# Kernel optimization log

Measured on AMD Instinct MI355X. Metric: run time of the kernel, lower is better.

The kernel has to match this reference:

```python
import jax, jax.numpy as jnp
import numpy as np

V, E, H, S, B = 32000, 512, 1024, 256, 128
D_WIN = 5.0  # local attention half-window D


def setup_inputs() -> dict:
    key = jax.random.key(0)
    ks = jax.random.split(key, 12)
    f32 = jnp.float32
    nrm = lambda k, shape, s=0.02: (s * jax.random.normal(k, shape, dtype=f32))
    x = jax.random.randint(ks[0], (1, B), 0, V)  # single decode step of token ids
    previous_hidden = jax.random.normal(ks[1], (1, B, H), dtype=f32)
    encoder_outputs = jax.random.normal(ks[2], (S, B, H), dtype=f32)
    lengths = jax.random.randint(ks[3], (B,), S // 2, S + 1)
    enc_masks = (jnp.arange(S)[:, None] < lengths[None, :]).astype(jnp.int32)  # (S,B)
    emb = nrm(ks[4], (V, E))
    W_dec = nrm(ks[5], (H, H)); b_dec = jnp.zeros((H,), f32)
    W_pos = nrm(ks[6], (H, H)); b_pos = jnp.zeros((H,), f32)
    w_proj = nrm(ks[7], (1, H))
    W_ih = nrm(ks[8], (3 * H, E + H)); b_ih = jnp.zeros((3 * H,), f32)
    W_hh = nrm(ks[9], (3 * H, H)); b_hh = jnp.zeros((3 * H,), f32)
    W_fc = nrm(ks[10], (V, E + 2 * H)); b_fc = jnp.zeros((V,), f32)
    return dict(x=x, previous_hidden=previous_hidden, encoder_outputs=encoder_outputs,
                enc_masks=enc_masks, emb=emb, W_dec=W_dec, b_dec=b_dec,
                W_pos=W_pos, b_pos=b_pos, w_proj=w_proj,
                W_ih=W_ih, b_ih=b_ih, W_hh=W_hh, b_hh=b_hh, W_fc=W_fc, b_fc=b_fc)


def reference(x, previous_hidden, encoder_outputs, enc_masks, emb, W_dec, b_dec,
              W_pos, b_pos, w_proj, W_ih, b_ih, W_hh, b_hh, W_fc, b_fc):
    src_len = encoder_outputs.shape[0]
    x_emb = emb[x]                                   # (1,B,E); dropout is eval-mode identity
    phd = previous_hidden[-1]                        # (B,H)

    # per-batch encoder lengths: first index where mask==0, 0 -> full length
    src_lens = jnp.argmin(enc_masks.T, axis=1)
    src_lens = jnp.where(src_lens == 0, src_len, src_lens).astype(jnp.float32)  # (B,)

    # local (Luong-style) alignment scores: tanh of dot(dec, enc)
    dw = phd @ W_dec.T + b_dec                       # (B,H)
    energy = jnp.tanh(jnp.einsum('bh,sbh->sb', dw, encoder_outputs))  # (S,B)
    scores = jnp.where(enc_masks == 0, -jnp.inf, energy)
    att_w = jax.nn.softmax(scores, axis=0)           # (S,B)

    # predicted center position pt = (len-1) * sigmoid(v^T tanh(W_p h))
    t = jnp.tanh(previous_hidden @ W_pos.T + b_pos)  # (1,B,H)
    f_ht = jax.nn.sigmoid(t @ w_proj.T)[0, :, 0]     # (B,)
    pt = (src_lens - 1.0) * f_ht                     # (B,)

    # Gaussian window centered at pt, sigma = D/2, plus hard [pmin,pmax) mask
    s = jnp.arange(src_len, dtype=jnp.float32)[:, None]          # (S,1)
    sigma = D_WIN / 2.0
    window = jnp.exp(-((pt[None, :] - s) ** 2) / (2.0 * sigma ** 2))  # (S,B)
    pmax = jnp.floor(pt + D_WIN)
    pmin = jnp.floor(jnp.maximum(pt - D_WIN, 0.0))
    hard = (s < pmax[None, :]) & (s >= pmin[None, :])
    window = window * hard.astype(window.dtype)
    w = att_w * window                               # (S,B), NOT renormalized (as in source)

    context = jnp.einsum('sb,sbh->bh', w, encoder_outputs)  # (B,H)

    # single GRU step (torch gate order: r, z, n)
    gru_in = jnp.concatenate([x_emb[0], context], axis=1)    # (B,E+H)
    gi = gru_in @ W_ih.T + b_ih                              # (B,3H)
    gh = phd @ W_hh.T + b_hh                                 # (B,3H)
    i_r, i_z, i_n = jnp.split(gi, 3, axis=1)
    h_r, h_z, h_n = jnp.split(gh, 3, axis=1)
    r = jax.nn.sigmoid(i_r + h_r)
    zg = jax.nn.sigmoid(i_z + h_z)
    n = jnp.tanh(i_n + r * h_n)
    h_new = (1.0 - zg) * n + zg * phd                        # (B,H)

    new_input = jnp.concatenate([x_emb, h_new[None], context[None]], axis=2)  # (1,B,E+2H)
    z = new_input @ W_fc.T + b_fc                            # (1,B,V)
    return z, h_new[None]
```

## Files before the change

### kernel.cpp

```cpp
#include <hip/hip_runtime.h>
#include <math.h>

#define B_ 128
#define S_ 256
#define H_ 1024
#define E_ 512
#define V_ 32000
#define KZ (E_ + 2 * H_)
#define NKB (KZ / 32)

typedef short s8v  __attribute__((ext_vector_type(8)));
typedef float f32x4 __attribute__((ext_vector_type(4)));
typedef unsigned short us4 __attribute__((ext_vector_type(4)));
typedef unsigned short us8 __attribute__((ext_vector_type(8)));

__device__ __forceinline__ unsigned short f2bf(float f)
{
    union { float f; unsigned u; } v; v.f = f;
    unsigned r = v.u + 0x7fffu + ((v.u >> 16) & 1u);
    return (unsigned short)(r >> 16);
}

__global__ __launch_bounds__(256) void prep_kernel(
    const int* __restrict__ x, const float* __restrict__ emb, float* __restrict__ x_emb,
    const float* __restrict__ b_dec, float* __restrict__ dwdec,
    const float* __restrict__ b_pos, float* __restrict__ dwpos,
    const float* __restrict__ b_ih, float* __restrict__ gi,
    const float* __restrict__ b_hh, float* __restrict__ gh)
{
    int idx = blockIdx.x * 256 + threadIdx.x;
    if (idx < B_ * E_) { x_emb[idx] = emb[(size_t)x[idx >> 9] * E_ + (idx & 511)]; return; }
    idx -= B_ * E_;
    if (idx < B_ * H_) { dwdec[idx] = b_dec[idx & 1023]; return; }
    idx -= B_ * H_;
    if (idx < B_ * H_) { dwpos[idx] = b_pos[idx & 1023]; return; }
    idx -= B_ * H_;
    if (idx < B_ * 3 * H_) { gi[idx] = b_ih[idx % (3 * H_)]; return; }
    idx -= B_ * 3 * H_;
    gh[idx] = b_hh[idx % (3 * H_)];
}

template<int TILE_N, int MICRO_N, bool ATOMIC, bool CONCAT>
__device__ __forceinline__ void gemm_core(const float* __restrict__ A,
                                          const float* __restrict__ Aa,
                                          const float* __restrict__ Ab,
                                          const float* __restrict__ W,
                                          const float* __restrict__ bias,
                                          float* __restrict__ C,
                                          int N, int K, int kbeg, int kend,
                                          float (*As)[132], float (*Ws)[TILE_N + 4])
{
    constexpr int NT_N   = TILE_N / MICRO_N;
    constexpr int NT_M   = 256 / NT_N;
    constexpr int MICRO_M = 128 / NT_M;
    const int tid = threadIdx.x;
    const int n0  = blockIdx.x * TILE_N;
    const int tn  = (tid % NT_N) * MICRO_N;
    const int tm  = (tid / NT_N) * MICRO_M;

    float acc[MICRO_M][MICRO_N] = {};

    for (int k0 = kbeg; k0 < kend; k0 += 16) {
        #pragma unroll
        for (int r = 0; r < 2; r++) {
            int v  = tid + 256 * r;
            int m  = v >> 2;
            int kk = (v & 3) << 2;
            int kcol = k0 + kk;
            float4 a4;
            if (CONCAT)
                a4 = (kcol < E_) ? *(const float4*)(Aa + (size_t)m * E_ + kcol)
                                 : *(const float4*)(Ab + (size_t)m * H_ + (kcol - E_));
            else
                a4 = *(const float4*)(A + (size_t)m * K + kcol);
            As[kk + 0][m] = a4.x; As[kk + 1][m] = a4.y;
            As[kk + 2][m] = a4.z; As[kk + 3][m] = a4.w;
        }
        for (int v = tid; v < TILE_N * 4; v += 256) {
            int n  = v >> 2;
            int kk = (v & 3) << 2;
            float4 w4 = *(const float4*)(W + (size_t)(n0 + n) * K + k0 + kk);
            Ws[kk + 0][n] = w4.x; Ws[kk + 1][n] = w4.y;
            Ws[kk + 2][n] = w4.z; Ws[kk + 3][n] = w4.w;
        }
        __syncthreads();
        #pragma unroll
        for (int kk = 0; kk < 16; kk++) {
            float a[MICRO_M], w[MICRO_N];
            #pragma unroll
            for (int i = 0; i < MICRO_M; i++) a[i] = As[kk][tm + i];
            #pragma unroll
            for (int j = 0; j < MICRO_N; j++) w[j] = Ws[kk][tn + j];
            #pragma unroll
            for (int i = 0; i < MICRO_M; i++)
                #pragma unroll
                for (int j = 0; j < MICRO_N; j++)
                    acc[i][j] = fmaf(a[i], w[j], acc[i][j]);
        }
        __syncthreads();
    }

    #pragma unroll
    for (int i = 0; i < MICRO_M; i++) {
        #pragma unroll
        for (int j = 0; j < MICRO_N; j++) {
            size_t off = (size_t)(tm + i) * N + n0 + tn + j;
            if (ATOMIC) atomicAdd(C + off, acc[i][j]);
            else        C[off] = acc[i][j] + bias[n0 + tn + j];
        }
    }
}

template<bool CONCAT0>
__global__ __launch_bounds__(256) void gemm_dual(const float* A0, const float* A0a, const float* A0b,
                                                 const float* W0, float* C0, int K0, int kc0,
                                                 const float* A1, const float* W1, float* C1, int K1, int kc1,
                                                 int N)
{
    __shared__ float As[16][132];
    __shared__ float Ws[16][36];
    if (blockIdx.z == 0)
        gemm_core<32, 2, true, CONCAT0>(A0, A0a, A0b, W0, nullptr, C0, N, K0,
                                        blockIdx.y * kc0, blockIdx.y * kc0 + kc0, As, Ws);
    else
        gemm_core<32, 2, true, false>(A1, nullptr, nullptr, W1, nullptr, C1, N, K1,
                                      blockIdx.y * kc1, blockIdx.y * kc1 + kc1, As, Ws);
}

__global__ __launch_bounds__(256) void gemm_z_mfma(const unsigned short* __restrict__ A2,
                                                   const float* __restrict__ W,
                                                   const float* __restrict__ bias,
                                                   float* __restrict__ C)
{
    __shared__ unsigned short Ws[4][64 * 40];

    const int tid  = threadIdx.x;
    const int n0   = blockIdx.x * 64;
    const int w    = tid >> 6;
    const int lane = tid & 63;
    const int quad = lane >> 4;
    const int l16  = lane & 15;

    const int sn0 = tid >> 3;
    const int sk  = (tid & 7) << 2;
    const float* wp0 = W + (size_t)(n0 + sn0) * KZ + sk;
    const float* wp1 = W + (size_t)(n0 + sn0 + 32) * KZ + sk;
    const int wsoff0 = sn0 * 40 + sk;
    const int wsoff1 = (sn0 + 32) * 40 + sk;
    const unsigned short* ap = A2 + lane * 8;
    const int boff = (w * 16 + l16) * 40 + quad * 8;

    float4 wA[2], wB[2];
    f32x4 acc[8] = {};

    auto ldw = [&](int kb, float4 (&r)[2]) {
        r[0] = *(const float4*)(wp0 + kb * 32);
        r[1] = *(const float4*)(wp1 + kb * 32);
    };
    auto stw = [&](int buf, const float4 (&r)[2]) {
        us4 p0, p1;
        p0.x = f2bf(r[0].x); p0.y = f2bf(r[0].y); p0.z = f2bf(r[0].z); p0.w = f2bf(r[0].w);
        p1.x = f2bf(r[1].x); p1.y = f2bf(r[1].y); p1.z = f2bf(r[1].z); p1.w = f2bf(r[1].w);
        *(us4*)&Ws[buf][wsoff0] = p0;
        *(us4*)&Ws[buf][wsoff1] = p1;
    };
    auto barrier = [&]() {
        asm volatile("s_waitcnt lgkmcnt(0)" ::: "memory");
        __builtin_amdgcn_s_barrier();
        asm volatile("" ::: "memory");
    };
    auto subiter = [&](int kb, float4 (&wLd)[2], const float4 (&wSt)[2]) {
        s8v af[8];
        const unsigned short* ab = ap + (size_t)kb * 4096;
        #pragma unroll
        for (int mt = 0; mt < 8; mt++) af[mt] = *(const s8v*)(ab + mt * 512);
        if (kb + 2 < NKB) ldw(kb + 2, wLd);
        s8v bfrag = *(const s8v*)&Ws[kb & 3][boff];
        #pragma unroll
        for (int mt = 0; mt < 8; mt++)
            acc[mt] = __builtin_amdgcn_mfma_f32_16x16x32_bf16(af[mt], bfrag, acc[mt], 0, 0, 0);
        if (kb + 1 < NKB) stw((kb + 1) & 3, wSt);
        barrier();
    };

    ldw(0, wA); ldw(1, wB);
    stw(0, wA);
    barrier();

    #pragma unroll 1
    for (int kb = 0; kb < NKB; kb += 2) {
        subiter(kb,     wA, wB);
        subiter(kb + 1, wB, wA);
    }

    const int n  = n0 + w * 16 + l16;
    const float bv = bias[n];
    #pragma unroll
    for (int mt = 0; mt < 8; mt++)
        #pragma unroll
        for (int r = 0; r < 4; r++)
            C[(size_t)(mt * 16 + quad * 4 + r) * V_ + n] = acc[mt][r] + bv;
}

__global__ __launch_bounds__(256) void pt_kernel(const int* __restrict__ masks,
                                                 const float* __restrict__ dwpos,
                                                 const float* __restrict__ w_proj,
                                                 float* __restrict__ pt)
{
    __shared__ int   smin_s[4];
    __shared__ float ssum[4];
    int b = blockIdx.x, tid = threadIdx.x;
    int lane = tid & 63, wv = tid >> 6;

    int first = (masks[tid * B_ + b] == 0) ? tid : S_;
    for (int off = 32; off; off >>= 1) first = min(first, __shfl_down(first, off, 64));
    if (lane == 0) smin_s[wv] = first;

    float sum = 0.f;
    for (int i = tid; i < H_; i += 256) sum += w_proj[i] * tanhf(dwpos[(size_t)b * H_ + i]);
    for (int off = 32; off; off >>= 1) sum += __shfl_down(sum, off, 64);
    if (lane == 0) ssum[wv] = sum;
    __syncthreads();
    if (tid == 0) {
        int   fz  = min(min(smin_s[0], smin_s[1]), min(smin_s[2], smin_s[3]));
        float tot = ssum[0] + ssum[1] + ssum[2] + ssum[3];
        float fht = 1.f / (1.f + expf(-tot));
        pt[b] = ((float)fz - 1.f) * fht;
    }
}

__global__ __launch_bounds__(256) void energy_kernel(const float* __restrict__ dw,
                                                     const float* __restrict__ enc,
                                                     const int* __restrict__ masks,
                                                     float* __restrict__ energy)
{
    int wid  = (blockIdx.x << 2) + (threadIdx.x >> 6);
    int lane = threadIdx.x & 63;
    int b    = wid & (B_ - 1);
    const float4* ep = (const float4*)(enc + (size_t)wid * H_);
    const float4* dp = (const float4*)(dw + (size_t)b * H_);
    float acc = 0.f;
    #pragma unroll
    for (int i = 0; i < 4; i++) {
        float4 a = dp[lane + (i << 6)];
        float4 e = ep[lane + (i << 6)];
        acc += a.x * e.x + a.y * e.y + a.z * e.z + a.w * e.w;
    }
    for (int off = 32; off; off >>= 1) acc += __shfl_down(acc, off, 64);
    if (lane == 0)
        energy[wid] = masks[wid] ? tanhf(acc) : -1e30f;
}

__global__ __launch_bounds__(256) void softmax_window(const float* __restrict__ energy,
                                                      const float* __restrict__ pt,
                                                      float* __restrict__ w_sb)
{
    __shared__ float sred[4];
    int b = blockIdx.x, s = threadIdx.x;
    int lane = s & 63, wv = s >> 6;
    float e = energy[s * B_ + b];

    float m = e;
    for (int off = 32; off; off >>= 1) m = fmaxf(m, __shfl_down(m, off, 64));
    if (lane == 0) sred[wv] = m;
    __syncthreads();
    m = fmaxf(fmaxf(sred[0], sred[1]), fmaxf(sred[2], sred[3]));
    __syncthreads();

    float ex = expf(e - m);
    float l = ex;
    for (int off = 32; off; off >>= 1) l += __shfl_down(l, off, 64);
    if (lane == 0) sred[wv] = l;
    __syncthreads();
    l = sred[0] + sred[1] + sred[2] + sred[3];

    float aw   = ex / l;
    float ptb  = pt[b];
    float fs   = (float)s;
    float pmax = floorf(ptb + 5.f);
    float pmin = floorf(fmaxf(ptb - 5.f, 0.f));
    float d    = ptb - fs;
    float win  = ((fs < pmax) && (fs >= pmin)) ? expf(-(d * d) * (1.f / 12.5f)) : 0.f;
    w_sb[s * B_ + b] = aw * win;
}

__global__ __launch_bounds__(256) void context_kernel(const float* __restrict__ w_sb,
                                                      const float* __restrict__ enc,
                                                      const float* __restrict__ pt,
                                                      float* __restrict__ ctx)
{
    int b = blockIdx.y;
    int h = blockIdx.x * 256 + threadIdx.x;
    float ptb = pt[b];
    int smin = (int)floorf(fmaxf(ptb - 5.f, 0.f));
    int smax = min((int)floorf(ptb + 5.f), S_);
    float acc = 0.f;
    for (int s = smin; s < smax; s++)
        acc += w_sb[s * B_ + b] * enc[(size_t)(s * B_ + b) * H_ + h];
    ctx[(size_t)b * H_ + h] = acc;
}

__global__ __launch_bounds__(256) void gru_concat(const float* __restrict__ x_emb,
                                                  const float* __restrict__ gi,
                                                  const float* __restrict__ gh,
                                                  const float* __restrict__ phd,
                                                  const float* __restrict__ ctx,
                                                  float* __restrict__ out_h,
                                                  unsigned short* __restrict__ A2)
{
    int gid = blockIdx.x * 256 + threadIdx.x;
    int l   = gid & 63;
    int mt  = (gid >> 6) & 7;
    int kb  = gid >> 9;
    int b   = mt * 16 + (l & 15);
    int k0  = kb * 32 + ((l >> 4) << 3);

    float v[8];
    if (k0 < E_) {
        const float* p = x_emb + (size_t)b * E_ + k0;
        #pragma unroll
        for (int j = 0; j < 8; j++) v[j] = p[j];
    } else if (k0 < E_ + H_) {
        int i0 = k0 - E_;
        const float* gib = gi + (size_t)b * 3 * H_ + i0;
        const float* ghb = gh + (size_t)b * 3 * H_ + i0;
        const float* ph  = phd + (size_t)b * H_ + i0;
        float* oh = out_h + (size_t)b * H_ + i0;
        #pragma unroll
        for (int j = 0; j < 8; j++) {
            float ir = gib[j], iz = gib[H_ + j], in_ = gib[2 * H_ + j];
            float hr = ghb[j], hz = ghb[H_ + j], hn  = ghb[2 * H_ + j];
            float r  = 1.f / (1.f + expf(-(ir + hr)));
            float zg = 1.f / (1.f + expf(-(iz + hz)));
            float n  = tanhf(in_ + r * hn);
            float h  = (1.f - zg) * n + zg * ph[j];
            oh[j] = h;
            v[j] = h;
        }
    } else {
        const float* p = ctx + (size_t)b * H_ + (k0 - E_ - H_);
        #pragma unroll
        for (int j = 0; j < 8; j++) v[j] = p[j];
    }
    us8 o;
    #pragma unroll
    for (int j = 0; j < 8; j++) o[j] = f2bf(v[j]);
    *(us8*)(A2 + (size_t)gid * 8) = o;
}

extern "C" void kernel_launch(void* const* d_in, const int* in_sizes, int n_in,
                              void* d_out, int out_size, void* d_ws, size_t ws_size,
                              hipStream_t stream)
{
    const int*   x      = (const int*)  d_in[0];
    const float* phd    = (const float*)d_in[1];
    const float* enc    = (const float*)d_in[2];
    const int*   masks  = (const int*)  d_in[3];
    const float* emb    = (const float*)d_in[4];
    const float* W_dec  = (const float*)d_in[5];
    const float* b_dec  = (const float*)d_in[6];
    const float* W_pos  = (const float*)d_in[7];
    const float* b_pos  = (const float*)d_in[8];
    const float* w_proj = (const float*)d_in[9];
    const float* W_ih   = (const float*)d_in[10];
    const float* b_ih   = (const float*)d_in[11];
    const float* W_hh   = (const float*)d_in[12];
    const float* b_hh   = (const float*)d_in[13];
    const float* W_fc   = (const float*)d_in[14];
    const float* b_fc   = (const float*)d_in[15];

    float* out_z = (float*)d_out;
    float* out_h = out_z + (size_t)B_ * V_;

    float* ws       = (float*)d_ws;
    float* x_emb    = ws;  ws += B_ * E_;
    float* dwdec    = ws;  ws += B_ * H_;
    float* dwpos    = ws;  ws += B_ * H_;
    float* pt       = ws;  ws += 128;
    float* energy   = ws;  ws += S_ * B_;
    float* w_sb     = ws;  ws += S_ * B_;
    float* ctx      = ws;  ws += B_ * H_;
    float* gi       = ws;  ws += B_ * 3 * H_;
    float* gh       = ws;  ws += B_ * 3 * H_;
    unsigned short* A2 = (unsigned short*)ws;

    prep_kernel<<<4352, 256, 0, stream>>>(x, emb, x_emb, b_dec, dwdec, b_pos, dwpos,
                                          b_ih, gi, b_hh, gh);

    gemm_dual<false><<<dim3(H_ / 32, 4, 2), 256, 0, stream>>>(
        phd, nullptr, nullptr, W_dec, dwdec, H_, 256,
        phd,                   W_pos, dwpos, H_, 256, H_);

    pt_kernel<<<B_, 256, 0, stream>>>(masks, dwpos, w_proj, pt);
    energy_kernel<<<S_ * B_ / 4, 256, 0, stream>>>(dwdec, enc, masks, energy);
    softmax_window<<<B_, 256, 0, stream>>>(energy, pt, w_sb);
    context_kernel<<<dim3(H_ / 256, B_), 256, 0, stream>>>(w_sb, enc, pt, ctx);

    gemm_dual<true><<<dim3(3 * H_ / 32, 4, 2), 256, 0, stream>>>(
        nullptr, x_emb, ctx, W_ih, gi, E_ + H_, 384,
        phd,                 W_hh, gh, H_,      256, 3 * H_);

    gru_concat<<<B_ * KZ / 8 / 256, 256, 0, stream>>>(x_emb, gi, gh, phd, ctx, out_h, A2);

    gemm_z_mfma<<<V_ / 64, 256, 0, stream>>>(A2, W_fc, b_fc, out_z);
}
```

Measured before the change: 711.4 us.

## Split output projection by K and overlap its parts with earlier GEMMs

The W_fc projection is split along K into the embedding part, the context part and the hidden part. The embedding and context slices now run as extra blocks inside the attention-projection GEMM kernel and the GRU-input GEMM kernel, and only the hidden slice waits for the GRU. The pt, softmax-window and context kernels are fused into one per-batch attention kernel that also writes bf16 context directly into the MFMA operand buffer. This cuts launches and overlaps the bandwidth-heavy W_fc streaming with the small GEMMs. The cost is extra read-modify-write passes over the 128x32000 output and more shared memory per block in the fused kernels.

```diff
diff --git a/kernel.cpp b/kernel.cpp
--- a/kernel.cpp
+++ b/kernel.cpp
@@ -7,7 +7,6 @@
 #define E_ 512
 #define V_ 32000
 #define KZ (E_ + 2 * H_)
-#define NKB (KZ / 32)
 
 typedef short s8v  __attribute__((ext_vector_type(8)));
 typedef float f32x4 __attribute__((ext_vector_type(4)));
@@ -26,7 +25,8 @@
     const float* __restrict__ b_dec, float* __restrict__ dwdec,
     const float* __restrict__ b_pos, float* __restrict__ dwpos,
     const float* __restrict__ b_ih, float* __restrict__ gi,
-    const float* __restrict__ b_hh, float* __restrict__ gh)
+    const float* __restrict__ b_hh, float* __restrict__ gh,
+    unsigned short* __restrict__ A2)
 {
     int idx = blockIdx.x * 256 + threadIdx.x;
     if (idx < B_ * E_) { x_emb[idx] = emb[(size_t)x[idx >> 9] * E_ + (idx & 511)]; return; }
@@ -37,24 +37,32 @@
     idx -= B_ * H_;
     if (idx < B_ * 3 * H_) { gi[idx] = b_ih[idx % (3 * H_)]; return; }
     idx -= B_ * 3 * H_;
-    gh[idx] = b_hh[idx % (3 * H_)];
-}
-
-template<int TILE_N, int MICRO_N, bool ATOMIC, bool CONCAT>
+    if (idx < B_ * 3 * H_) { gh[idx] = b_hh[idx % (3 * H_)]; return; }
+    idx -= B_ * 3 * H_;
+    int l  = idx & 63;
+    int mt = (idx >> 6) & 7;
+    int b  = mt * 16 + (l & 15);
+    int k0 = (idx >> 9) * 32 + ((l >> 4) << 3);
+    const float* p = emb + (size_t)x[b] * E_ + k0;
+    us8 o;
+    #pragma unroll
+    for (int j = 0; j < 8; j++) o[j] = f2bf(p[j]);
+    *(us8*)(A2 + (size_t)idx * 8) = o;
+}
+
+template<int TILE_N, int MICRO_N, bool CONCAT>
 __device__ __forceinline__ void gemm_core(const float* __restrict__ A,
                                           const float* __restrict__ Aa,
                                           const float* __restrict__ Ab,
                                           const float* __restrict__ W,
-                                          const float* __restrict__ bias,
                                           float* __restrict__ C,
-                                          int N, int K, int kbeg, int kend,
+                                          int N, int K, int kbeg, int kend, int n0,
                                           float (*As)[132], float (*Ws)[TILE_N + 4])
 {
     constexpr int NT_N   = TILE_N / MICRO_N;
     constexpr int NT_M   = 256 / NT_N;
     constexpr int MICRO_M = 128 / NT_M;
     const int tid = threadIdx.x;
-    const int n0  = blockIdx.x * TILE_N;
     const int tn  = (tid % NT_N) * MICRO_N;
     const int tm  = (tid / NT_N) * MICRO_M;
 
@@ -101,41 +109,21 @@
     }
 
     #pragma unroll
-    for (int i = 0; i < MICRO_M; i++) {
-        #pragma unroll
-        for (int j = 0; j < MICRO_N; j++) {
-            size_t off = (size_t)(tm + i) * N + n0 + tn + j;
-            if (ATOMIC) atomicAdd(C + off, acc[i][j]);
-            else        C[off] = acc[i][j] + bias[n0 + tn + j];
-        }
-    }
-}
-
-template<bool CONCAT0>
-__global__ __launch_bounds__(256) void gemm_dual(const float* A0, const float* A0a, const float* A0b,
-                                                 const float* W0, float* C0, int K0, int kc0,
-                                                 const float* A1, const float* W1, float* C1, int K1, int kc1,
-                                                 int N)
-{
-    __shared__ float As[16][132];
-    __shared__ float Ws[16][36];
-    if (blockIdx.z == 0)
-        gemm_core<32, 2, true, CONCAT0>(A0, A0a, A0b, W0, nullptr, C0, N, K0,
-                                        blockIdx.y * kc0, blockIdx.y * kc0 + kc0, As, Ws);
-    else
-        gemm_core<32, 2, true, false>(A1, nullptr, nullptr, W1, nullptr, C1, N, K1,
-                                      blockIdx.y * kc1, blockIdx.y * kc1 + kc1, As, Ws);
-}
-
-__global__ __launch_bounds__(256) void gemm_z_mfma(const unsigned short* __restrict__ A2,
-                                                   const float* __restrict__ W,
-                                                   const float* __restrict__ bias,
-                                                   float* __restrict__ C)
-{
-    __shared__ unsigned short Ws[4][64 * 40];
-
+    for (int i = 0; i < MICRO_M; i++)
+        #pragma unroll
+        for (int j = 0; j < MICRO_N; j++)
+            atomicAdd(C + (size_t)(tm + i) * N + n0 + tn + j, acc[i][j]);
+}
+
+__device__ __forceinline__ void zpart(const unsigned short* __restrict__ A2,
+                                      const float* __restrict__ W,
+                                      const float* __restrict__ bias,
+                                      float* __restrict__ C,
+                                      int blk, int kb0, int nkb, bool first,
+                                      unsigned short (*Ws)[2560])
+{
     const int tid  = threadIdx.x;
-    const int n0   = blockIdx.x * 64;
+    const int n0   = blk * 64;
     const int w    = tid >> 6;
     const int lane = tid & 63;
     const int quad = lane >> 4;
@@ -143,19 +131,19 @@
 
     const int sn0 = tid >> 3;
     const int sk  = (tid & 7) << 2;
-    const float* wp0 = W + (size_t)(n0 + sn0) * KZ + sk;
-    const float* wp1 = W + (size_t)(n0 + sn0 + 32) * KZ + sk;
+    const float* wp0 = W + (size_t)(n0 + sn0) * KZ + kb0 * 32 + sk;
+    const float* wp1 = W + (size_t)(n0 + sn0 + 32) * KZ + kb0 * 32 + sk;
     const int wsoff0 = sn0 * 40 + sk;
     const int wsoff1 = (sn0 + 32) * 40 + sk;
-    const unsigned short* ap = A2 + lane * 8;
+    const unsigned short* ap = A2 + (size_t)kb0 * 4096 + lane * 8;
     const int boff = (w * 16 + l16) * 40 + quad * 8;
 
     float4 wA[2], wB[2];
     f32x4 acc[8] = {};
 
-    auto ldw = [&](int kb, float4 (&r)[2]) {
-        r[0] = *(const float4*)(wp0 + kb * 32);
-        r[1] = *(const float4*)(wp1 + kb * 32);
+    auto ldw = [&](int t, float4 (&r)[2]) {
+        r[0] = *(const float4*)(wp0 + t * 32);
+        r[1] = *(const float4*)(wp1 + t * 32);
     };
     auto stw = [&](int buf, const float4 (&r)[2]) {
         us4 p0, p1;
@@ -169,17 +157,17 @@
         __builtin_amdgcn_s_barrier();
         asm volatile("" ::: "memory");
     };
-    auto subiter = [&](int kb, float4 (&wLd)[2], const float4 (&wSt)[2]) {
+    auto subiter = [&](int t, float4 (&wLd)[2], const float4 (&wSt)[2]) {
         s8v af[8];
-        const unsigned short* ab = ap + (size_t)kb * 4096;
+        const unsigned short* ab = ap + (size_t)t * 4096;
         #pragma unroll
         for (int mt = 0; mt < 8; mt++) af[mt] = *(const s8v*)(ab + mt * 512);
-        if (kb + 2 < NKB) ldw(kb + 2, wLd);
-        s8v bfrag = *(const s8v*)&Ws[kb & 3][boff];
+        if (t + 2 < nkb) ldw(t + 2, wLd);
+        s8v bfrag = *(const s8v*)&Ws[t & 3][boff];
         #pragma unroll
         for (int mt = 0; mt < 8; mt++)
             acc[mt] = __builtin_amdgcn_mfma_f32_16x16x32_bf16(af[mt], bfrag, acc[mt], 0, 0, 0);
-        if (kb + 1 < NKB) stw((kb + 1) & 3, wSt);
+        if (t + 1 < nkb) stw((t + 1) & 3, wSt);
         barrier();
     };
 
@@ -188,45 +176,82 @@
     barrier();
 
     #pragma unroll 1
-    for (int kb = 0; kb < NKB; kb += 2) {
-        subiter(kb,     wA, wB);
-        subiter(kb + 1, wB, wA);
-    }
-
-    const int n  = n0 + w * 16 + l16;
-    const float bv = bias[n];
-    #pragma unroll
-    for (int mt = 0; mt < 8; mt++)
-        #pragma unroll
-        for (int r = 0; r < 4; r++)
-            C[(size_t)(mt * 16 + quad * 4 + r) * V_ + n] = acc[mt][r] + bv;
-}
-
-__global__ __launch_bounds__(256) void pt_kernel(const int* __restrict__ masks,
-                                                 const float* __restrict__ dwpos,
-                                                 const float* __restrict__ w_proj,
-                                                 float* __restrict__ pt)
-{
-    __shared__ int   smin_s[4];
-    __shared__ float ssum[4];
-    int b = blockIdx.x, tid = threadIdx.x;
-    int lane = tid & 63, wv = tid >> 6;
-
-    int first = (masks[tid * B_ + b] == 0) ? tid : S_;
-    for (int off = 32; off; off >>= 1) first = min(first, __shfl_down(first, off, 64));
-    if (lane == 0) smin_s[wv] = first;
-
-    float sum = 0.f;
-    for (int i = tid; i < H_; i += 256) sum += w_proj[i] * tanhf(dwpos[(size_t)b * H_ + i]);
-    for (int off = 32; off; off >>= 1) sum += __shfl_down(sum, off, 64);
-    if (lane == 0) ssum[wv] = sum;
-    __syncthreads();
-    if (tid == 0) {
-        int   fz  = min(min(smin_s[0], smin_s[1]), min(smin_s[2], smin_s[3]));
-        float tot = ssum[0] + ssum[1] + ssum[2] + ssum[3];
-        float fht = 1.f / (1.f + expf(-tot));
-        pt[b] = ((float)fz - 1.f) * fht;
-    }
+    for (int t = 0; t < nkb; t += 2) {
+        subiter(t,     wA, wB);
+        subiter(t + 1, wB, wA);
+    }
+
+    const int n = n0 + w * 16 + l16;
+    if (first) {
+        const float bv = bias[n];
+        #pragma unroll
+        for (int mt = 0; mt < 8; mt++)
+            #pragma unroll
+            for (int r = 0; r < 4; r++)
+                C[(size_t)(mt * 16 + quad * 4 + r) * V_ + n] = acc[mt][r] + bv;
+    } else {
+        #pragma unroll
+        for (int mt = 0; mt < 8; mt++)
+            #pragma unroll
+            for (int r = 0; r < 4; r++)
+                C[(size_t)(mt * 16 + quad * 4 + r) * V_ + n] += acc[mt][r];
+    }
+}
+
+__global__ __launch_bounds__(256) void fused_d1z1(
+    const float* __restrict__ phd,
+    const float* __restrict__ W_dec, float* __restrict__ dwdec,
+    const float* __restrict__ W_pos, float* __restrict__ dwpos,
+    const unsigned short* __restrict__ A2, const float* __restrict__ W_fc,
+    const float* __restrict__ b_fc, float* __restrict__ out_z)
+{
+    __shared__ float As[16][132];
+    __shared__ float Wsf[16][36];
+    __shared__ unsigned short Wz[4][2560];
+    int id = blockIdx.x;
+    if (id < 256) {
+        int xb = id & 31, yb = (id >> 5) & 3, zb = id >> 7;
+        if (zb == 0)
+            gemm_core<32, 2, false>(phd, nullptr, nullptr, W_dec, dwdec, H_, H_,
+                                    yb * 256, yb * 256 + 256, xb * 32, As, Wsf);
+        else
+            gemm_core<32, 2, false>(phd, nullptr, nullptr, W_pos, dwpos, H_, H_,
+                                    yb * 256, yb * 256 + 256, xb * 32, As, Wsf);
+    } else {
+        zpart(A2, W_fc, b_fc, out_z, id - 256, 0, 16, true, Wz);
+    }
+}
+
+__global__ __launch_bounds__(256) void fused_d2z3(
+    const float* __restrict__ x_emb, const float* __restrict__ ctx,
+    const float* __restrict__ W_ih, float* __restrict__ gi,
+    const float* __restrict__ phd, const float* __restrict__ W_hh, float* __restrict__ gh,
+    const unsigned short* __restrict__ A2, const float* __restrict__ W_fc,
+    float* __restrict__ out_z)
+{
+    __shared__ float As[16][132];
+    __shared__ float Wsf[16][36];
+    __shared__ unsigned short Wz[4][2560];
+    int id = blockIdx.x;
+    if (id < 768) {
+        int xb = id % 96, yb = (id / 96) & 3, zb = id / 384;
+        if (zb == 0)
+            gemm_core<32, 2, true>(nullptr, x_emb, ctx, W_ih, gi, 3 * H_, E_ + H_,
+                                   yb * 384, yb * 384 + 384, xb * 32, As, Wsf);
+        else
+            gemm_core<32, 2, false>(phd, nullptr, nullptr, W_hh, gh, 3 * H_, H_,
+                                    yb * 256, yb * 256 + 256, xb * 32, As, Wsf);
+    } else {
+        zpart(A2, W_fc, nullptr, out_z, id - 768, 48, 32, false, Wz);
+    }
+}
+
+__global__ __launch_bounds__(256) void zpart_kernel(const unsigned short* __restrict__ A2,
+                                                    const float* __restrict__ W_fc,
+                                                    float* __restrict__ out_z)
+{
+    __shared__ unsigned short Wz[4][2560];
+    zpart(A2, W_fc, nullptr, out_z, blockIdx.x, 16, 32, false, Wz);
 }
 
 __global__ __launch_bounds__(256) void energy_kernel(const float* __restrict__ dw,
@@ -251,22 +276,45 @@
         energy[wid] = masks[wid] ? tanhf(acc) : -1e30f;
 }
 
-__global__ __launch_bounds__(256) void softmax_window(const float* __restrict__ energy,
-                                                      const float* __restrict__ pt,
-                                                      float* __restrict__ w_sb)
+__global__ __launch_bounds__(256) void attn2(const float* __restrict__ energy,
+                                             const int* __restrict__ masks,
+                                             const float* __restrict__ dwpos,
+                                             const float* __restrict__ w_proj,
+                                             const float* __restrict__ enc,
+                                             float* __restrict__ ctx,
+                                             unsigned short* __restrict__ A2)
 {
     __shared__ float sred[4];
-    int b = blockIdx.x, s = threadIdx.x;
-    int lane = s & 63, wv = s >> 6;
-    float e = energy[s * B_ + b];
-
+    __shared__ int   sredi[4];
+    __shared__ float w_lds[S_];
+    __shared__ float ctx_lds[H_];
+    __shared__ float s_pt;
+    int b = blockIdx.x, tid = threadIdx.x;
+    int lane = tid & 63, wv = tid >> 6;
+
+    int first = (masks[tid * B_ + b] == 0) ? tid : S_;
+    for (int off = 32; off; off >>= 1) first = min(first, __shfl_down(first, off, 64));
+    if (lane == 0) sredi[wv] = first;
+    float sum = 0.f;
+    for (int i = tid; i < H_; i += 256) sum += w_proj[i] * tanhf(dwpos[(size_t)b * H_ + i]);
+    for (int off = 32; off; off >>= 1) sum += __shfl_down(sum, off, 64);
+    if (lane == 0) sred[wv] = sum;
+    __syncthreads();
+    if (tid == 0) {
+        int   fz  = min(min(sredi[0], sredi[1]), min(sredi[2], sredi[3]));
+        float tot = sred[0] + sred[1] + sred[2] + sred[3];
+        s_pt = ((float)fz - 1.f) * (1.f / (1.f + expf(-tot)));
+    }
+    __syncthreads();
+    float ptb = s_pt;
+
+    float e = energy[tid * B_ + b];
     float m = e;
     for (int off = 32; off; off >>= 1) m = fmaxf(m, __shfl_down(m, off, 64));
     if (lane == 0) sred[wv] = m;
     __syncthreads();
     m = fmaxf(fmaxf(sred[0], sred[1]), fmaxf(sred[2], sred[3]));
     __syncthreads();
-
     float ex = expf(e - m);
     float l = ex;
     for (int off = 32; off; off >>= 1) l += __shfl_down(l, off, 64);
@@ -274,78 +322,66 @@
     __syncthreads();
     l = sred[0] + sred[1] + sred[2] + sred[3];
 
-    float aw   = ex / l;
-    float ptb  = pt[b];
-    float fs   = (float)s;
+    float fs   = (float)tid;
     float pmax = floorf(ptb + 5.f);
     float pmin = floorf(fmaxf(ptb - 5.f, 0.f));
     float d    = ptb - fs;
     float win  = ((fs < pmax) && (fs >= pmin)) ? expf(-(d * d) * (1.f / 12.5f)) : 0.f;
-    w_sb[s * B_ + b] = aw * win;
-}
-
-__global__ __launch_bounds__(256) void context_kernel(const float* __restrict__ w_sb,
-                                                      const float* __restrict__ enc,
-                                                      const float* __restrict__ pt,
-                                                      float* __restrict__ ctx)
-{
-    int b = blockIdx.y;
-    int h = blockIdx.x * 256 + threadIdx.x;
-    float ptb = pt[b];
+    w_lds[tid] = (ex / l) * win;
+    __syncthreads();
+
     int smin = (int)floorf(fmaxf(ptb - 5.f, 0.f));
     int smax = min((int)floorf(ptb + 5.f), S_);
-    float acc = 0.f;
-    for (int s = smin; s < smax; s++)
-        acc += w_sb[s * B_ + b] * enc[(size_t)(s * B_ + b) * H_ + h];
-    ctx[(size_t)b * H_ + h] = acc;
-}
-
-__global__ __launch_bounds__(256) void gru_concat(const float* __restrict__ x_emb,
-                                                  const float* __restrict__ gi,
+    for (int h = tid; h < H_; h += 256) {
+        float acc = 0.f;
+        for (int s = smin; s < smax; s++)
+            acc += w_lds[s] * enc[((size_t)s * B_ + b) * H_ + h];
+        ctx[(size_t)b * H_ + h] = acc;
+        ctx_lds[h] = acc;
+    }
+    __syncthreads();
+
+    if (tid < 128) {
+        int kb = 48 + (tid >> 2);
+        int hi = tid & 3;
+        int i0 = (tid >> 2) * 32 + hi * 8;
+        us8 o;
+        #pragma unroll
+        for (int j = 0; j < 8; j++) o[j] = f2bf(ctx_lds[i0 + j]);
+        *(us8*)(A2 + ((size_t)(kb * 8 + (b >> 4)) * 64 + hi * 16 + (b & 15)) * 8) = o;
+    }
+}
+
+__global__ __launch_bounds__(256) void gru_concat(const float* __restrict__ gi,
                                                   const float* __restrict__ gh,
                                                   const float* __restrict__ phd,
-                                                  const float* __restrict__ ctx,
                                                   float* __restrict__ out_h,
                                                   unsigned short* __restrict__ A2)
 {
     int gid = blockIdx.x * 256 + threadIdx.x;
     int l   = gid & 63;
     int mt  = (gid >> 6) & 7;
-    int kb  = gid >> 9;
+    int kbr = gid >> 9;
     int b   = mt * 16 + (l & 15);
-    int k0  = kb * 32 + ((l >> 4) << 3);
-
-    float v[8];
-    if (k0 < E_) {
-        const float* p = x_emb + (size_t)b * E_ + k0;
-        #pragma unroll
-        for (int j = 0; j < 8; j++) v[j] = p[j];
-    } else if (k0 < E_ + H_) {
-        int i0 = k0 - E_;
-        const float* gib = gi + (size_t)b * 3 * H_ + i0;
-        const float* ghb = gh + (size_t)b * 3 * H_ + i0;
-        const float* ph  = phd + (size_t)b * H_ + i0;
-        float* oh = out_h + (size_t)b * H_ + i0;
-        #pragma unroll
-        for (int j = 0; j < 8; j++) {
-            float ir = gib[j], iz = gib[H_ + j], in_ = gib[2 * H_ + j];
-            float hr = ghb[j], hz = ghb[H_ + j], hn  = ghb[2 * H_ + j];
-            float r  = 1.f / (1.f + expf(-(ir + hr)));
-            float zg = 1.f / (1.f + expf(-(iz + hz)));
-            float n  = tanhf(in_ + r * hn);
-            float h  = (1.f - zg) * n + zg * ph[j];
-            oh[j] = h;
-            v[j] = h;
-        }
-    } else {
-        const float* p = ctx + (size_t)b * H_ + (k0 - E_ - H_);
-        #pragma unroll
-        for (int j = 0; j < 8; j++) v[j] = p[j];
-    }
+    int i0  = kbr * 32 + ((l >> 4) << 3);
+
+    const float* gib = gi + (size_t)b * 3 * H_ + i0;
+    const float* ghb = gh + (size_t)b * 3 * H_ + i0;
+    const float* ph  = phd + (size_t)b * H_ + i0;
+    float* oh = out_h + (size_t)b * H_ + i0;
     us8 o;
     #pragma unroll
-    for (int j = 0; j < 8; j++) o[j] = f2bf(v[j]);
-    *(us8*)(A2 + (size_t)gid * 8) = o;
+    for (int j = 0; j < 8; j++) {
+        float ir = gib[j], iz = gib[H_ + j], in_ = gib[2 * H_ + j];
+        float hr = ghb[j], hz = ghb[H_ + j], hn  = ghb[2 * H_ + j];
+        float r  = 1.f / (1.f + expf(-(ir + hr)));
+        float zg = 1.f / (1.f + expf(-(iz + hz)));
+        float n  = tanhf(in_ + r * hn);
+        float h  = (1.f - zg) * n + zg * ph[j];
+        oh[j] = h;
+        o[j] = f2bf(h);
+    }
+    *(us8*)(A2 + (size_t)(8192 + gid) * 8) = o;
 }
 
 extern "C" void kernel_launch(void* const* d_in, const int* in_sizes, int n_in,
@@ -376,31 +412,26 @@
     float* x_emb    = ws;  ws += B_ * E_;
     float* dwdec    = ws;  ws += B_ * H_;
     float* dwpos    = ws;  ws += B_ * H_;
-    float* pt       = ws;  ws += 128;
     float* energy   = ws;  ws += S_ * B_;
-    float* w_sb     = ws;  ws += S_ * B_;
     float* ctx      = ws;  ws += B_ * H_;
     float* gi       = ws;  ws += B_ * 3 * H_;
     float* gh       = ws;  ws += B_ * 3 * H_;
     unsigned short* A2 = (unsigned short*)ws;
 
-    prep_kernel<<<4352, 256, 0, stream>>>(x, emb, x_emb, b_dec, dwdec, b_pos, dwpos,
-                                          b_ih, gi, b_hh, gh);
-
-    gemm_dual<false><<<dim3(H_ / 32, 4, 2), 256, 0, stream>>>(
-        phd, nullptr, nullptr, W_dec, dwdec, H_, 256,
-        phd,                   W_pos, dwpos, H_, 256, H_);
-
-    pt_kernel<<<B_, 256, 0, stream>>>(masks, dwpos, w_proj, pt);
+    prep_kernel<<<4384, 256, 0, stream>>>(x, emb, x_emb, b_dec, dwdec, b_pos, dwpos,
+                                          b_ih, gi, b_hh, gh, A2);
+
+    fused_d1z1<<<756, 256, 0, stream>>>(phd, W_dec, dwdec, W_pos, dwpos,
+                                        A2, W_fc, b_fc, out_z);
+
     energy_kernel<<<S_ * B_ / 4, 256, 0, stream>>>(dwdec, enc, masks, energy);
-    softmax_window<<<B_, 256, 0, stream>>>(energy, pt, w_sb);
-    context_kernel<<<dim3(H_ / 256, B_), 256, 0, stream>>>(w_sb, enc, pt, ctx);
-
-    gemm_dual<true><<<dim3(3 * H_ / 32, 4, 2), 256, 0, stream>>>(
-        nullptr, x_emb, ctx, W_ih, gi, E_ + H_, 384,
-        phd,                 W_hh, gh, H_,      256, 3 * H_);
-
-    gru_concat<<<B_ * KZ / 8 / 256, 256, 0, stream>>>(x_emb, gi, gh, phd, ctx, out_h, A2);
-
-    gemm_z_mfma<<<V_ / 64, 256, 0, stream>>>(A2, W_fc, b_fc, out_z);
-}
+
+    attn2<<<B_, 256, 0, stream>>>(energy, masks, dwpos, w_proj, enc, ctx, A2);
+
+    fused_d2z3<<<1268, 256, 0, stream>>>(x_emb, ctx, W_ih, gi, phd, W_hh, gh,
+                                         A2, W_fc, out_z);
+
+    gru_concat<<<64, 256, 0, stream>>>(gi, gh, phd, out_h, A2);
+
+    zpart_kernel<<<500, 256, 0, stream>>>(A2, W_fc, out_z);
+}
```

Measured after the change: 723.2 us. No clear change (+1.6%).
